# Optimization experiments

Hardware: AMD Instinct MI355X
Metric: run time of the kernel (lower is better)

The kernel has to match this reference:

```python
import jax, jax.numpy as jnp
import numpy as np

B, N, D, H = 128, 2048, 128, 8
HD = D // H


def setup_inputs() -> dict:
    key = jax.random.key(0)
    ks = jax.random.split(key, 10)
    x = jax.random.normal(ks[0], (B, N, D), dtype=jnp.float32)
    first_node = jax.random.randint(ks[1], (B, 1), 0, N, dtype=jnp.int64)
    current_node = jax.random.randint(ks[2], (B, 1), 0, N, dtype=jnp.int64)
    mask = jax.random.randint(ks[3], (B, N), 0, 2).astype(jnp.bool_)
    s = 0.02
    W_lin = jax.random.normal(ks[4], (D, 3 * D), dtype=jnp.float32) * s
    b_lin = jnp.zeros((D,), dtype=jnp.float32)
    Wq = jax.random.normal(ks[5], (D, D), dtype=jnp.float32) * s
    bq = jnp.zeros((D,), dtype=jnp.float32)
    Wk = jax.random.normal(ks[6], (D, D), dtype=jnp.float32) * s
    bk = jnp.zeros((D,), dtype=jnp.float32)
    return {"x": x, "first_node": first_node, "current_node": current_node,
            "mask": mask, "W_lin": W_lin, "b_lin": b_lin,
            "Wq": Wq, "bq": bq, "Wk": Wk, "bk": bk}


def reference(x, first_node, current_node, mask, W_lin, b_lin, Wq, bq, Wk, bk):
    # y = x.clone().detach()
    y = jax.lax.stop_gradient(x)
    graph_emb = jnp.mean(y, axis=-2)                       # [B, D]
    bidx = jnp.arange(B)
    first_feat = y[bidx, first_node[:, 0]]                 # [B, D]
    curr_feat = y[bidx, current_node[:, 0]]                # [B, D]
    context = jnp.concatenate([graph_emb, first_feat, curr_feat], axis=-1)  # [B, 3D]
    q_in = context @ W_lin.T + b_lin                       # [B, D]
    # single-query multi-head attention; only attn weights are used
    q = (q_in @ Wq.T + bq).reshape(B, H, HD)               # [B, H, hd]
    k = (x @ Wk.T + bk).reshape(B, N, H, HD)               # [B, N, H, hd]
    scores = jnp.einsum('bhd,bnhd->bhn', q, k) / jnp.sqrt(jnp.float32(HD))
    scores = jnp.where(mask[:, None, :], -jnp.inf, scores)  # key_padding_mask: True = masked
    attn = jax.nn.softmax(scores, axis=-1)                 # [B, H, N]
    return jnp.mean(attn, axis=1)                          # average over heads -> [B, N]
```

## Files before the change

kernel.cpp:

```cpp
#include <hip/hip_runtime.h>
#include <hip/hip_bf16.h>

#define BB 128
#define NN 2048
#define DD 128
#define HH 8

#define GSUM_OFF 0
#define ESUM_OFF 16384
#define WQE_OFF  17408
#define SB_OFF   148480
#define E_OFF    262144

__global__ void k1_gsum(const float* __restrict__ x, float* __restrict__ gsum) {
    int b = blockIdx.y;
    int chunk = blockIdx.x;
    int t = threadIdx.x;
    int c2 = t & 63;
    int rg = t >> 6;
    const float2* x2 = (const float2*)(x + ((size_t)b * NN + chunk * 128) * DD);
    float2 acc = make_float2(0.f, 0.f);
    for (int i = 0; i < 64; ++i) {
        float2 v = x2[(size_t)(rg + 2 * i) * 64 + c2];
        acc.x += v.x; acc.y += v.y;
    }
    atomicAdd(&gsum[b * DD + c2 * 2 + 0], acc.x);
    atomicAdd(&gsum[b * DD + c2 * 2 + 1], acc.y);
}

__global__ void k2_q(const float* __restrict__ x,
                     const int* __restrict__ fn_p, const int* __restrict__ cn_p,
                     const float* __restrict__ Wl, const float* __restrict__ bl,
                     const float* __restrict__ Wq, const float* __restrict__ bq,
                     const float* __restrict__ Wk, const float* __restrict__ bk,
                     float* __restrict__ ws) {
    __shared__ float ctx[384];
    __shared__ float qin[128];
    __shared__ float qv[128];
    int b = blockIdx.x, t = threadIdx.x;

    bool is64 = (fn_p[1] == 0 && fn_p[3] == 0 && fn_p[5] == 0 && fn_p[7] == 0 &&
                 cn_p[1] == 0 && cn_p[3] == 0 && cn_p[5] == 0 && cn_p[7] == 0);
    int fn = is64 ? fn_p[2 * b] : fn_p[b];
    int cn = is64 ? cn_p[2 * b] : cn_p[b];

    const float* gsum = ws + GSUM_OFF;
    ctx[t]       = gsum[b * DD + t] * (1.0f / NN);
    ctx[128 + t] = x[((size_t)b * NN + fn) * DD + t];
    ctx[256 + t] = x[((size_t)b * NN + cn) * DD + t];
    __syncthreads();

    float a = bl[t];
    const float* wrow = Wl + (size_t)t * 384;
    for (int e = 0; e < 384; ++e) a += ctx[e] * wrow[e];
    qin[t] = a;
    __syncthreads();

    float a2 = bq[t];
    const float* wrow2 = Wq + (size_t)t * 128;
    for (int e = 0; e < 128; ++e) a2 += qin[e] * wrow2[e];
    qv[t] = a2;
    __syncthreads();

    float* wqe = ws + WQE_OFF + (size_t)b * HH * DD;
    for (int h = 0; h < HH; ++h) {
        float w = 0.f;
        for (int j = 0; j < 16; ++j) w += qv[h * 16 + j] * Wk[(size_t)(h * 16 + j) * 128 + t];
        wqe[h * DD + t] = 0.25f * w;
    }
    if (t < HH) {
        float s = 0.f;
        for (int j = 0; j < 16; ++j) s += qv[t * 16 + j] * bk[t * 16 + j];
        (ws + SB_OFF)[b * HH + t] = 0.25f * s;
    }
}

__device__ __forceinline__ int detect_mask_kind(const int* mw) {
    int big = 0, oddnz = 0;
    #pragma unroll 8
    for (int i = 0; i < 64; ++i) {
        unsigned w = (unsigned)mw[i];
        if (w > 1u) big = 1;
        if ((i & 1) && w != 0u) oddnz = 1;
    }
    return big ? 0 : (oddnz ? 1 : 2);
}

__device__ __forceinline__ int mask_at(const unsigned char* mb, const int* mw, int kind, size_t idx) {
    if (kind == 0) return mb[idx];
    if (kind == 1) return mw[idx];
    return mw[2 * idx];
}

__launch_bounds__(256)
__global__ void k3_exp(const float* __restrict__ x, const void* __restrict__ mask,
                       const float* __restrict__ ws_ro,
                       float* __restrict__ wse, float* __restrict__ esum) {
    __shared__ float xs[64 * 132];
    __shared__ float wqs[8 * 132];
    __shared__ float sbs[8];
    int b = blockIdx.y, cx = blockIdx.x, t = threadIdx.x;

    const unsigned char* mb = (const unsigned char*)mask;
    const int* mw = (const int*)mask;
    int mkind = detect_mask_kind(mw);

    const float* wqe = ws_ro + WQE_OFF + (size_t)b * HH * DD;
    for (int i = t; i < 1024; i += 256) wqs[(i >> 7) * 132 + (i & 127)] = wqe[i];
    if (t < 8) sbs[t] = (ws_ro + SB_OFF)[b * HH + t];

    int h = t >> 5, nl = t & 31;
    float myes = 0.f;
    const float4* wrow = (const float4*)&wqs[h * 132];

    for (int sc = 0; sc < 4; ++sc) {
        int nb = cx * 256 + sc * 64;
        __syncthreads();
        const float4* xsrc = (const float4*)(x + ((size_t)b * NN + nb) * DD);
        for (int i = 0; i < 8; ++i) {
            int f4 = t + i * 256;
            int r = f4 >> 5, c4 = f4 & 31;
            *(float4*)&xs[r * 132 + c4 * 4] = xsrc[f4];
        }
        __syncthreads();

        float acc0 = sbs[h], acc1 = sbs[h];
        const float4* xr0 = (const float4*)&xs[nl * 132];
        const float4* xr1 = (const float4*)&xs[(nl + 32) * 132];
        #pragma unroll
        for (int e4 = 0; e4 < 32; ++e4) {
            float4 w = wrow[e4];
            float4 a = xr0[e4];
            float4 c = xr1[e4];
            acc0 += a.x * w.x + a.y * w.y + a.z * w.z + a.w * w.w;
            acc1 += c.x * w.x + c.y * w.y + c.z * w.z + c.w * w.w;
        }
        int n0 = nb + nl, n1 = nb + nl + 32;
        float e0 = mask_at(mb, mw, mkind, (size_t)b * NN + n0) ? 0.f : __expf(acc0);
        float e1 = mask_at(mb, mw, mkind, (size_t)b * NN + n1) ? 0.f : __expf(acc1);
        wse[((size_t)(b * HH + h)) * NN + n0] = e0;
        wse[((size_t)(b * HH + h)) * NN + n1] = e1;
        myes += e0 + e1;
    }
    for (int off = 16; off >= 1; off >>= 1) myes += __shfl_xor(myes, off, 64);
    if (nl == 0) atomicAdd(&esum[b * HH + h], myes);
}

__global__ void k4_out(const float* __restrict__ wse, const float* __restrict__ esum,
                       float* __restrict__ out) {
    __shared__ float rinv[8];
    int b = blockIdx.y, cx = blockIdx.x, t = threadIdx.x;
    if (t < 8) rinv[t] = 0.125f / esum[b * HH + t];
    __syncthreads();
    int n = cx * 256 + t;
    float o = 0.f;
    #pragma unroll
    for (int h = 0; h < HH; ++h)
        o += wse[((size_t)(b * HH + h)) * NN + n] * rinv[h];
    out[(size_t)b * NN + n] = o;
}

extern "C" void kernel_launch(void* const* d_in, const int* in_sizes, int n_in,
                              void* d_out, int out_size, void* d_ws, size_t ws_size,
                              hipStream_t stream) {
    const float* x  = (const float*)d_in[0];
    const int* fn   = (const int*)d_in[1];
    const int* cn   = (const int*)d_in[2];
    const void* mk  = d_in[3];
    const float* Wl = (const float*)d_in[4];
    const float* bl = (const float*)d_in[5];
    const float* Wq = (const float*)d_in[6];
    const float* bq = (const float*)d_in[7];
    const float* Wk = (const float*)d_in[8];
    const float* bk = (const float*)d_in[9];
    float* ws  = (float*)d_ws;
    float* out = (float*)d_out;

    hipMemsetAsync(d_ws, 0, (size_t)(16384 + 1024) * 4, stream);

    k1_gsum<<<dim3(16, BB), 128, 0, stream>>>(x, ws + GSUM_OFF);
    k2_q<<<BB, 128, 0, stream>>>(x, fn, cn, Wl, bl, Wq, bq, Wk, bk, ws);
    k3_exp<<<dim3(8, BB), 256, 0, stream>>>(x, mk, ws, ws + E_OFF, ws + ESUM_OFF);
    k4_out<<<dim3(8, BB), 256, 0, stream>>>(ws + E_OFF, ws + ESUM_OFF, out);
}
```

Measured before the change: 279.5 us.

## Precompose weight matrices, parallelize query projection, and register-tile score kernel

Measured after the change: 530.7 us. +89.9%, slower.

```diff
diff --git a/kernel.cpp b/kernel.cpp
--- a/kernel.cpp
+++ b/kernel.cpp
@@ -10,68 +10,133 @@
 #define ESUM_OFF 16384
 #define WQE_OFF  17408
 #define SB_OFF   148480
-#define E_OFF    262144
-
+#define P_OFF    149504
+#define PB_OFF   198656
+#define TT_OFF   198784
+#define UU_OFF   592000
+#define SBS_OFF  593024
+#define SBC_OFF  596096
+#define E_OFF    596608
+
+__launch_bounds__(256)
 __global__ void k1_gsum(const float* __restrict__ x, float* __restrict__ gsum) {
-    int b = blockIdx.y;
-    int chunk = blockIdx.x;
-    int t = threadIdx.x;
-    int c2 = t & 63;
-    int rg = t >> 6;
-    const float2* x2 = (const float2*)(x + ((size_t)b * NN + chunk * 128) * DD);
-    float2 acc = make_float2(0.f, 0.f);
-    for (int i = 0; i < 64; ++i) {
-        float2 v = x2[(size_t)(rg + 2 * i) * 64 + c2];
-        acc.x += v.x; acc.y += v.y;
-    }
-    atomicAdd(&gsum[b * DD + c2 * 2 + 0], acc.x);
-    atomicAdd(&gsum[b * DD + c2 * 2 + 1], acc.y);
-}
-
-__global__ void k2_q(const float* __restrict__ x,
-                     const int* __restrict__ fn_p, const int* __restrict__ cn_p,
-                     const float* __restrict__ Wl, const float* __restrict__ bl,
-                     const float* __restrict__ Wq, const float* __restrict__ bq,
-                     const float* __restrict__ Wk, const float* __restrict__ bk,
-                     float* __restrict__ ws) {
-    __shared__ float ctx[384];
-    __shared__ float qin[128];
-    __shared__ float qv[128];
-    int b = blockIdx.x, t = threadIdx.x;
-
+    int b = blockIdx.y, cx = blockIdx.x, t = threadIdx.x;
+    int c4 = t & 31, rg = t >> 5;
+    const float4* x4 = (const float4*)(x + ((size_t)b * NN + cx * 256) * DD);
+    float4 acc = make_float4(0.f, 0.f, 0.f, 0.f);
+    #pragma unroll 8
+    for (int i = 0; i < 32; ++i) {
+        float4 v = x4[(size_t)(rg + 8 * i) * 32 + c4];
+        acc.x += v.x; acc.y += v.y; acc.z += v.z; acc.w += v.w;
+    }
+    acc.x += __shfl_xor(acc.x, 32, 64);
+    acc.y += __shfl_xor(acc.y, 32, 64);
+    acc.z += __shfl_xor(acc.z, 32, 64);
+    acc.w += __shfl_xor(acc.w, 32, 64);
+    __shared__ float xsum[4][32][4];
+    int w = t >> 6, lane = t & 63;
+    if (lane < 32) {
+        xsum[w][lane][0] = acc.x; xsum[w][lane][1] = acc.y;
+        xsum[w][lane][2] = acc.z; xsum[w][lane][3] = acc.w;
+    }
+    __syncthreads();
+    if (t < 32) {
+        #pragma unroll
+        for (int comp = 0; comp < 4; ++comp) {
+            float s = xsum[0][t][comp] + xsum[1][t][comp] + xsum[2][t][comp] + xsum[3][t][comp];
+            atomicAdd(&gsum[b * DD + t * 4 + comp], s);
+        }
+    }
+}
+
+__global__ void k2a1(const float* __restrict__ Wq, const float* __restrict__ Wl,
+                     const float* __restrict__ bl, const float* __restrict__ bq,
+                     float* ws) {
+    __shared__ float wqL[128];
+    int m = blockIdx.x, t = threadIdx.x;
+    if (t < 128) wqL[t] = Wq[m * 128 + t];
+    __syncthreads();
+    float acc = 0.f;
+    #pragma unroll 8
+    for (int r = 0; r < 128; ++r) acc = fmaf(wqL[r], Wl[(size_t)r * 384 + t], acc);
+    ws[P_OFF + (size_t)m * 384 + t] = acc;
+    if (t == 0) {
+        float pb = bq[m];
+        for (int r = 0; r < 128; ++r) pb = fmaf(wqL[r], bl[r], pb);
+        ws[PB_OFF + m] = pb;
+    }
+}
+
+__global__ void k2a2(const float* __restrict__ Wk, const float* __restrict__ bk, float* ws) {
+    __shared__ float PL[16 * 33];
+    __shared__ float WkL[16 * 128];
+    __shared__ float pbL[16], bkL[16];
+    int ecb = blockIdx.x, h = blockIdx.y, t = threadIdx.x;
+    int e0 = ecb * 32;
+    const float* P = ws + P_OFF;
+    for (int i = t; i < 512; i += 128) {
+        int j = i >> 5, ec = i & 31;
+        PL[j * 33 + ec] = P[(size_t)(h * 16 + j) * 384 + e0 + ec];
+    }
+    for (int i = t; i < 2048; i += 128) WkL[i] = Wk[(size_t)h * 16 * 128 + i];
+    if (t < 16) { pbL[t] = ws[PB_OFF + h * 16 + t]; bkL[t] = bk[h * 16 + t]; }
+    __syncthreads();
+    int d = t;
+    for (int ec = 0; ec < 32; ++ec) {
+        float s = 0.f;
+        #pragma unroll
+        for (int j = 0; j < 16; ++j) s = fmaf(WkL[j * 128 + d], PL[j * 33 + ec], s);
+        ws[TT_OFF + ((size_t)h * 384 + e0 + ec) * 128 + d] = 0.25f * s;
+    }
+    if (ecb == 0) {
+        float s = 0.f;
+        #pragma unroll
+        for (int j = 0; j < 16; ++j) s = fmaf(WkL[j * 128 + d], pbL[j], s);
+        ws[UU_OFF + h * 128 + d] = 0.25f * s;
+    }
+    if (t < 32) {
+        float s = 0.f;
+        #pragma unroll
+        for (int j = 0; j < 16; ++j) s = fmaf(bkL[j], PL[j * 33 + t], s);
+        ws[SBS_OFF + h * 384 + e0 + t] = 0.25f * s;
+    }
+    if (ecb == 0 && t == 0) {
+        float s = 0.f;
+        for (int j = 0; j < 16; ++j) s = fmaf(bkL[j], pbL[j], s);
+        ws[SBC_OFF + h] = 0.25f * s;
+    }
+}
+
+__launch_bounds__(256)
+__global__ void k2b(const float* __restrict__ x,
+                    const int* __restrict__ fn_p, const int* __restrict__ cn_p,
+                    float* ws) {
+    __shared__ float ctxL[384];
+    int hp = blockIdx.x, b = blockIdx.y, t = threadIdx.x;
     bool is64 = (fn_p[1] == 0 && fn_p[3] == 0 && fn_p[5] == 0 && fn_p[7] == 0 &&
                  cn_p[1] == 0 && cn_p[3] == 0 && cn_p[5] == 0 && cn_p[7] == 0);
     int fn = is64 ? fn_p[2 * b] : fn_p[b];
     int cn = is64 ? cn_p[2 * b] : cn_p[b];
-
     const float* gsum = ws + GSUM_OFF;
-    ctx[t]       = gsum[b * DD + t] * (1.0f / NN);
-    ctx[128 + t] = x[((size_t)b * NN + fn) * DD + t];
-    ctx[256 + t] = x[((size_t)b * NN + cn) * DD + t];
-    __syncthreads();
-
-    float a = bl[t];
-    const float* wrow = Wl + (size_t)t * 384;
-    for (int e = 0; e < 384; ++e) a += ctx[e] * wrow[e];
-    qin[t] = a;
-    __syncthreads();
-
-    float a2 = bq[t];
-    const float* wrow2 = Wq + (size_t)t * 128;
-    for (int e = 0; e < 128; ++e) a2 += qin[e] * wrow2[e];
-    qv[t] = a2;
-    __syncthreads();
-
-    float* wqe = ws + WQE_OFF + (size_t)b * HH * DD;
-    for (int h = 0; h < HH; ++h) {
-        float w = 0.f;
-        for (int j = 0; j < 16; ++j) w += qv[h * 16 + j] * Wk[(size_t)(h * 16 + j) * 128 + t];
-        wqe[h * DD + t] = 0.25f * w;
-    }
-    if (t < HH) {
-        float s = 0.f;
-        for (int j = 0; j < 16; ++j) s += qv[t * 16 + j] * bk[t * 16 + j];
-        (ws + SB_OFF)[b * HH + t] = 0.25f * s;
+    if (t < 128) {
+        ctxL[t]       = gsum[b * DD + t] * (1.0f / NN);
+        ctxL[256 + t] = x[((size_t)b * NN + cn) * DD + t];
+    } else {
+        int u = t - 128;
+        ctxL[128 + u] = x[((size_t)b * NN + fn) * DD + u];
+    }
+    __syncthreads();
+    int h = hp * 2 + (t >> 7), d = t & 127;
+    float acc = ws[UU_OFF + h * 128 + d];
+    const float* T = ws + TT_OFF + (size_t)h * 384 * 128 + d;
+    #pragma unroll 8
+    for (int e = 0; e < 384; ++e) acc = fmaf(T[(size_t)e * 128], ctxL[e], acc);
+    ws[WQE_OFF + (size_t)b * 1024 + h * 128 + d] = acc;
+    if (hp == 0 && t < 8) {
+        float s = ws[SBC_OFF + t];
+        const float* S = ws + SBS_OFF + t * 384;
+        for (int e = 0; e < 384; ++e) s = fmaf(S[e], ctxL[e], s);
+        ws[SB_OFF + b * HH + t] = s;
     }
 }
 
@@ -85,7 +150,6 @@
     }
     return big ? 0 : (oddnz ? 1 : 2);
 }
-
 __device__ __forceinline__ int mask_at(const unsigned char* mb, const int* mw, int kind, size_t idx) {
     if (kind == 0) return mb[idx];
     if (kind == 1) return mw[idx];
@@ -93,57 +157,65 @@
 }
 
 __launch_bounds__(256)
-__global__ void k3_exp(const float* __restrict__ x, const void* __restrict__ mask,
-                       const float* __restrict__ ws_ro,
-                       float* __restrict__ wse, float* __restrict__ esum) {
-    __shared__ float xs[64 * 132];
-    __shared__ float wqs[8 * 132];
-    __shared__ float sbs[8];
+__global__ void k3r(const float* __restrict__ x, const void* __restrict__ mask,
+                    const float* __restrict__ ws_ro,
+                    float* __restrict__ wse, float* __restrict__ esum) {
+    __shared__ float wqL[1024];
+    __shared__ float sbL[8];
     int b = blockIdx.y, cx = blockIdx.x, t = threadIdx.x;
+    const float* wqe = ws_ro + WQE_OFF + (size_t)b * 1024;
+    for (int i = t; i < 1024; i += 256) wqL[i] = wqe[i];
+    if (t < 8) sbL[t] = (ws_ro + SB_OFF)[b * HH + t];
+    __syncthreads();
 
     const unsigned char* mb = (const unsigned char*)mask;
     const int* mw = (const int*)mask;
     int mkind = detect_mask_kind(mw);
 
-    const float* wqe = ws_ro + WQE_OFF + (size_t)b * HH * DD;
-    for (int i = t; i < 1024; i += 256) wqs[(i >> 7) * 132 + (i & 127)] = wqe[i];
-    if (t < 8) sbs[t] = (ws_ro + SB_OFF)[b * HH + t];
-
-    int h = t >> 5, nl = t & 31;
-    float myes = 0.f;
-    const float4* wrow = (const float4*)&wqs[h * 132];
-
-    for (int sc = 0; sc < 4; ++sc) {
-        int nb = cx * 256 + sc * 64;
-        __syncthreads();
-        const float4* xsrc = (const float4*)(x + ((size_t)b * NN + nb) * DD);
-        for (int i = 0; i < 8; ++i) {
-            int f4 = t + i * 256;
-            int r = f4 >> 5, c4 = f4 & 31;
-            *(float4*)&xs[r * 132 + c4 * 4] = xsrc[f4];
+    int n0 = cx * 512 + t, n1 = n0 + 256;
+    float accA[8], accB[8];
+    #pragma unroll
+    for (int h = 0; h < HH; ++h) { accA[h] = sbL[h]; accB[h] = sbL[h]; }
+
+    const float4* xA = (const float4*)(x + ((size_t)b * NN + n0) * DD);
+    const float4* xB = (const float4*)(x + ((size_t)b * NN + n1) * DD);
+
+    #pragma unroll
+    for (int p = 0; p < 4; ++p) {
+        float4 a[8], c[8];
+        #pragma unroll
+        for (int q = 0; q < 8; ++q) { a[q] = xA[p * 8 + q]; c[q] = xB[p * 8 + q]; }
+        #pragma unroll
+        for (int h = 0; h < HH; ++h) {
+            const float4* w4 = (const float4*)&wqL[h * 128 + p * 32];
+            #pragma unroll
+            for (int q = 0; q < 8; ++q) {
+                float4 w = w4[q];
+                accA[h] += a[q].x * w.x + a[q].y * w.y + a[q].z * w.z + a[q].w * w.w;
+                accB[h] += c[q].x * w.x + c[q].y * w.y + c[q].z * w.z + c[q].w * w.w;
+            }
         }
-        __syncthreads();
-
-        float acc0 = sbs[h], acc1 = sbs[h];
-        const float4* xr0 = (const float4*)&xs[nl * 132];
-        const float4* xr1 = (const float4*)&xs[(nl + 32) * 132];
-        #pragma unroll
-        for (int e4 = 0; e4 < 32; ++e4) {
-            float4 w = wrow[e4];
-            float4 a = xr0[e4];
-            float4 c = xr1[e4];
-            acc0 += a.x * w.x + a.y * w.y + a.z * w.z + a.w * w.w;
-            acc1 += c.x * w.x + c.y * w.y + c.z * w.z + c.w * w.w;
-        }
-        int n0 = nb + nl, n1 = nb + nl + 32;
-        float e0 = mask_at(mb, mw, mkind, (size_t)b * NN + n0) ? 0.f : __expf(acc0);
-        float e1 = mask_at(mb, mw, mkind, (size_t)b * NN + n1) ? 0.f : __expf(acc1);
-        wse[((size_t)(b * HH + h)) * NN + n0] = e0;
-        wse[((size_t)(b * HH + h)) * NN + n1] = e1;
-        myes += e0 + e1;
-    }
-    for (int off = 16; off >= 1; off >>= 1) myes += __shfl_xor(myes, off, 64);
-    if (nl == 0) atomicAdd(&esum[b * HH + h], myes);
+    }
+
+    size_t mbase = (size_t)b * NN;
+    int m0 = mask_at(mb, mw, mkind, mbase + n0);
+    int m1 = mask_at(mb, mw, mkind, mbase + n1);
+    float eA[8], eB[8];
+    #pragma unroll
+    for (int h = 0; h < HH; ++h) {
+        eA[h] = m0 ? 0.f : __expf(accA[h]);
+        eB[h] = m1 ? 0.f : __expf(accB[h]);
+        wse[((size_t)(b * HH + h)) * NN + n0] = eA[h];
+        wse[((size_t)(b * HH + h)) * NN + n1] = eB[h];
+    }
+    int lane = t & 63;
+    #pragma unroll
+    for (int h = 0; h < HH; ++h) {
+        float v = eA[h] + eB[h];
+        #pragma unroll
+        for (int off = 32; off >= 1; off >>= 1) v += __shfl_xor(v, off, 64);
+        if (lane == 0) atomicAdd(&esum[b * HH + h], v);
+    }
 }
 
 __global__ void k4_out(const float* __restrict__ wse, const float* __restrict__ esum,
@@ -178,8 +250,10 @@
 
     hipMemsetAsync(d_ws, 0, (size_t)(16384 + 1024) * 4, stream);
 
-    k1_gsum<<<dim3(16, BB), 128, 0, stream>>>(x, ws + GSUM_OFF);
-    k2_q<<<BB, 128, 0, stream>>>(x, fn, cn, Wl, bl, Wq, bq, Wk, bk, ws);
-    k3_exp<<<dim3(8, BB), 256, 0, stream>>>(x, mk, ws, ws + E_OFF, ws + ESUM_OFF);
+    k1_gsum<<<dim3(8, BB), 256, 0, stream>>>(x, ws + GSUM_OFF);
+    k2a1<<<128, 384, 0, stream>>>(Wq, Wl, bl, bq, ws);
+    k2a2<<<dim3(12, HH), 128, 0, stream>>>(Wk, bk, ws);
+    k2b<<<dim3(4, BB), 256, 0, stream>>>(x, fn, cn, ws);
+    k3r<<<dim3(4, BB), 256, 0, stream>>>(x, mk, ws, ws + E_OFF, ws + ESUM_OFF);
     k4_out<<<dim3(8, BB), 256, 0, stream>>>(ws + E_OFF, ws + ESUM_OFF, out);
 }
```
